# Performance work log

Hardware: AMD Instinct MI355X
Metric: run time of the kernel (lower is better)

## Reference

```python
import jax, jax.numpy as jnp
import numpy as np

N_SAMPLES = 16_777_216  # total surviving samples across all rays
N_RAY = 65_536          # number of rays


def setup_inputs() -> dict:
    key = jax.random.key(0)
    k1, k2 = jax.random.split(key)
    alpha = jax.random.uniform(k1, (N_SAMPLES,), dtype=jnp.float32)
    # sorted ray ids -> contiguous segments, as produced by create_full_step_id + masking
    ray_id = jnp.sort(jax.random.randint(k2, (N_SAMPLES,), 0, N_RAY, dtype=jnp.int32))
    return {"alpha": alpha, "ray_id": ray_id, "N_ray": N_RAY}


def _seg_prod_op(a, b):
    # segmented-product combine: reset the running product at segment starts
    va, fa = a
    vb, fb = b
    return jnp.where(fb, vb, va * vb), fa | fb


def reference(alpha, ray_id, N_ray):
    n = alpha.shape[0]
    one_minus_alpha = 1.0 - alpha + 1e-11                      # [n]
    is_start = jnp.concatenate(
        [jnp.ones((1,), jnp.bool_), ray_id[1:] != ray_id[:-1]]
    )                                                          # [n] segment starts
    # parallel segmented cumulative product (replaces the per-sample Python loop)
    cumprod, _ = jax.lax.associative_scan(_seg_prod_op, (one_minus_alpha, is_start))
    # NOTE: faithful to the source: transmittance is a global shift of cumprod
    # (cat([1, cumprod[:-1]])), NOT reset to 1 at each ray start.
    transmittance = jnp.concatenate([jnp.ones((1,), alpha.dtype), cumprod[:-1]])
    weights = alpha * transmittance                            # [n]
    # last sample index of each ray (ids are sorted, so max index == last write)
    last_idx = jnp.zeros((N_ray,), jnp.int32).at[ray_id].max(
        jnp.arange(n, dtype=jnp.int32)
    )                                                          # [N_ray]
    alphainv_last = cumprod[last_idx]                          # [N_ray]
    return weights, alphainv_last
```

## Files before the change

kernel.cpp:

```cpp
#include <hip/hip_runtime.h>
#include <stdint.h>


#define BLOCK 256
#define NWAVE (BLOCK / 64)
#define NJ 4
#define WELEM (64 * 4 * NJ)
#define CHUNK (NWAVE * WELEM)
#define LOOKW 1024

struct Pair { float v; int f; };

__device__ __forceinline__ Pair seg_combine(Pair a, Pair b) {
    Pair r;
    r.v = b.f ? b.v : (a.v * b.v);
    r.f = a.f | b.f;
    return r;
}

__device__ __forceinline__ Pair wave_scan_incl(Pair x, int lane) {
    #pragma unroll
    for (int off = 1; off < 64; off <<= 1) {
        Pair o;
        o.v = __shfl_up(x.v, off);
        o.f = __shfl_up(x.f, off);
        if (lane >= off) x = seg_combine(o, x);
    }
    return x;
}

__global__ void nerf_init(const float* __restrict__ alpha,
                          float* __restrict__ alphainv, int N_ray) {
    int i = blockIdx.x * blockDim.x + threadIdx.x;
    if (i < N_ray) alphainv[i] = (1.0f - alpha[0]) + 1e-11f;
}

__global__ __launch_bounds__(BLOCK, 4)
void nerf_fused(const float* __restrict__ alpha, const int* __restrict__ ray_id,
                float* __restrict__ weights, float* __restrict__ alphainv, int n) {
    __shared__ float s_wv[NWAVE];
    __shared__ int   s_wf[NWAVE];
    __shared__ int   s_rid[BLOCK];
    __shared__ float s_bv;
    __shared__ int   s_bf;

    const int c = blockIdx.x, t = threadIdx.x;
    const int lane = t & 63, w = t >> 6;
    const long bstart = (long)c * CHUNK;
    const long wbase  = bstart + (long)w * WELEM;

    float P0 = 1.0f;
    if (c > 0) {
        long wlo = bstart - LOOKW;
        Pair chain; chain.v = 1.0f; chain.f = 0;
        for (;;) {
            const long e0 = wlo + 4 * t;
            float4 av = *(const float4*)(alpha  + e0);
            int4   rv = *(const int4*)  (ray_id + e0);
            s_rid[t] = rv.w;
            __syncthreads();
            const int prev = (t == 0) ? ((wlo > 0) ? ray_id[wlo - 1] : -1) : s_rid[t - 1];
            Pair l;
            l.v = (1.0f - av.x) + 1e-11f; l.f = (rv.x != prev);
            { Pair e; e.v = (1.0f - av.y) + 1e-11f; e.f = (rv.y != rv.x); l = seg_combine(l, e); }
            { Pair e; e.v = (1.0f - av.z) + 1e-11f; e.f = (rv.z != rv.y); l = seg_combine(l, e); }
            { Pair e; e.v = (1.0f - av.w) + 1e-11f; e.f = (rv.w != rv.z); l = seg_combine(l, e); }
            #pragma unroll
            for (int off = 1; off < 64; off <<= 1) {
                Pair o;
                o.v = __shfl_down(l.v, off);
                o.f = __shfl_down(l.f, off);
                l = seg_combine(l, o);
            }
            if (lane == 0) { s_wv[w] = l.v; s_wf[w] = l.f; }
            __syncthreads();
            if (t == 0) {
                Pair acc; acc.v = s_wv[0]; acc.f = s_wf[0];
                #pragma unroll
                for (int ww = 1; ww < NWAVE; ++ww) {
                    Pair e; e.v = s_wv[ww]; e.f = s_wf[ww];
                    acc = seg_combine(acc, e);
                }
                s_bv = acc.v; s_bf = acc.f;
            }
            __syncthreads();
            Pair wagg; wagg.v = s_bv; wagg.f = s_bf;
            chain = seg_combine(wagg, chain);
            if (chain.f || wlo == 0) break;
            wlo -= LOOKW;
        }
        P0 = chain.v;
    }

    int last_r = -1;
    if (wbase > 0 && wbase - 1 < (long)n) last_r = ray_id[wbase - 1];

    float4 A[NJ]; int4 R[NJ]; Pair E[NJ]; int PR0[NJ];
    Pair wrun; wrun.v = 1.0f; wrun.f = 0;

    #pragma unroll
    for (int j = 0; j < NJ; ++j) {
        const long e0 = wbase + j * 256 + lane * 4;
        if (e0 + 4 <= (long)n) {
            A[j] = *(const float4*)(alpha  + e0);
            R[j] = *(const int4*)  (ray_id + e0);
        } else {
            float aa[4]; int rr[4];
            for (int k = 0; k < 4; ++k) {
                long g = e0 + k;
                aa[k] = (g < n) ? alpha[g]  : 0.0f;
                rr[k] = (g < n) ? ray_id[g] : -2;
            }
            A[j] = make_float4(aa[0], aa[1], aa[2], aa[3]);
            R[j] = make_int4(rr[0], rr[1], rr[2], rr[3]);
        }
        const float4 av = A[j]; const int4 rv = R[j];
        const bool b0 = e0 < n, b1 = e0 + 1 < n, b2 = e0 + 2 < n, b3 = e0 + 3 < n;
        const float om0 = b0 ? (1.0f - av.x) + 1e-11f : 1.0f;
        const float om1 = b1 ? (1.0f - av.y) + 1e-11f : 1.0f;
        const float om2 = b2 ? (1.0f - av.z) + 1e-11f : 1.0f;
        const float om3 = b3 ? (1.0f - av.w) + 1e-11f : 1.0f;
        const int up = __shfl_up(rv.w, 1);
        const int prev0 = (lane == 0) ? last_r : up;
        PR0[j] = prev0;
        const int f0 = b0 && (rv.x != prev0);
        const int f1 = b1 && (rv.y != rv.x);
        const int f2 = b2 && (rv.z != rv.y);
        const int f3 = b3 && (rv.w != rv.z);

        Pair l; l.v = om0; l.f = f0;
        { Pair e; e.v = om1; e.f = f1; l = seg_combine(l, e); }
        { Pair e; e.v = om2; e.f = f2; l = seg_combine(l, e); }
        { Pair e; e.v = om3; e.f = f3; l = seg_combine(l, e); }

        Pair ws = wave_scan_incl(l, lane);
        Pair wse;
        {
            float uv = __shfl_up(ws.v, 1);
            int   uf = __shfl_up(ws.f, 1);
            if (lane == 0) { wse.v = 1.0f; wse.f = 0; }
            else           { wse.v = uv;   wse.f = uf; }
        }
        E[j] = seg_combine(wrun, wse);
        Pair jag; jag.v = __shfl(ws.v, 63); jag.f = __shfl(ws.f, 63);
        wrun = seg_combine(wrun, jag);
        last_r = __shfl(rv.w, 63);
    }

    if (lane == 0) { s_wv[w] = wrun.v; s_wf[w] = wrun.f; }
    __syncthreads();

    Pair base; base.v = P0; base.f = (c > 0);
    for (int ww = 0; ww < w; ++ww) {
        Pair e; e.v = s_wv[ww]; e.f = s_wf[ww];
        base = seg_combine(base, e);
    }

    #pragma unroll
    for (int j = 0; j < NJ; ++j) {
        Pair P = seg_combine(base, E[j]);
        const float4 av = A[j]; const int4 rv = R[j];
        const long e0 = wbase + j * 256 + lane * 4;
        const bool b0 = e0 < n, b1 = e0 + 1 < n, b2 = e0 + 2 < n, b3 = e0 + 3 < n;
        const float om0 = b0 ? (1.0f - av.x) + 1e-11f : 1.0f;
        const float om1 = b1 ? (1.0f - av.y) + 1e-11f : 1.0f;
        const float om2 = b2 ? (1.0f - av.z) + 1e-11f : 1.0f;
        const float om3 = b3 ? (1.0f - av.w) + 1e-11f : 1.0f;
        const int prev0 = PR0[j];
        const int f0 = b0 && (rv.x != prev0);
        const int f1 = b1 && (rv.y != rv.x);
        const int f2 = b2 && (rv.z != rv.y);
        const int f3 = b3 && (rv.w != rv.z);

        float w0, w1, w2, w3;
        w0 = av.x * P.v;
        if (f0 && e0 > 0) alphainv[prev0] = P.v;
        { Pair e; e.v = om0; e.f = f0; P = seg_combine(P, e); }
        if (b0 && e0 == (long)n - 1) alphainv[rv.x] = P.v;
        w1 = av.y * P.v;
        if (f1) alphainv[rv.x] = P.v;
        { Pair e; e.v = om1; e.f = f1; P = seg_combine(P, e); }
        if (b1 && e0 + 1 == (long)n - 1) alphainv[rv.y] = P.v;
        w2 = av.z * P.v;
        if (f2) alphainv[rv.y] = P.v;
        { Pair e; e.v = om2; e.f = f2; P = seg_combine(P, e); }
        if (b2 && e0 + 2 == (long)n - 1) alphainv[rv.z] = P.v;
        w3 = av.w * P.v;
        if (f3) alphainv[rv.z] = P.v;
        { Pair e; e.v = om3; e.f = f3; P = seg_combine(P, e); }
        if (b3 && e0 + 3 == (long)n - 1) alphainv[rv.w] = P.v;

        if (e0 + 4 <= (long)n) {
            *(float4*)(weights + e0) = make_float4(w0, w1, w2, w3);
        } else {
            float ww4[4] = {w0, w1, w2, w3};
            for (int k = 0; k < 4; ++k) {
                long g = e0 + k;
                if (g < n) weights[g] = ww4[k];
            }
        }
    }
}

extern "C" void kernel_launch(void* const* d_in, const int* in_sizes, int n_in,
                              void* d_out, int out_size, void* d_ws, size_t ws_size,
                              hipStream_t stream) {
    const float* alpha  = (const float*)d_in[0];
    const int*   ray_id = (const int*)d_in[1];
    const int n     = in_sizes[0];
    const int N_ray = out_size - n;

    float* weights  = (float*)d_out;
    float* alphainv = weights + n;

    const int nchunks = (n + CHUNK - 1) / CHUNK;

    nerf_init<<<(N_ray + BLOCK - 1) / BLOCK, BLOCK, 0, stream>>>(alpha, alphainv, N_ray);
    nerf_fused<<<nchunks, BLOCK, 0, stream>>>(alpha, ray_id, weights, alphainv, n);
}
```

Before: 179.3 us.

## Encode segment flag in float sign bit and use wave-level lookback

Packs each (value, segment-start flag) pair into one float by storing the flag in the sign bit. Each scan step then needs one shuffle instead of two, and fewer registers. The block-wide lookback with shared memory and three barriers becomes a per-wave lookback over a 256-element window, with no barriers, that every wave computes redundantly. The main-chunk loads are hoisted ahead of the lookback so their latency overlaps it. The risk is more redundant lookback loads per wave, and relying on the one-minus-alpha values always being positive.

```diff
diff --git a/kernel.cpp b/kernel.cpp
--- a/kernel.cpp
+++ b/kernel.cpp
@@ -7,26 +7,10 @@
 #define NJ 4
 #define WELEM (64 * 4 * NJ)
 #define CHUNK (NWAVE * WELEM)
-#define LOOKW 1024
+#define WIN 256
 
-struct Pair { float v; int f; };
-
-__device__ __forceinline__ Pair seg_combine(Pair a, Pair b) {
-    Pair r;
-    r.v = b.f ? b.v : (a.v * b.v);
-    r.f = a.f | b.f;
-    return r;
-}
-
-__device__ __forceinline__ Pair wave_scan_incl(Pair x, int lane) {
-    #pragma unroll
-    for (int off = 1; off < 64; off <<= 1) {
-        Pair o;
-        o.v = __shfl_up(x.v, off);
-        o.f = __shfl_up(x.f, off);
-        if (lane >= off) x = seg_combine(o, x);
-    }
-    return x;
+__device__ __forceinline__ float comb(float a, float b) {
+    return (__float_as_int(b) < 0) ? b : a * b;
 }
 
 __global__ void nerf_init(const float* __restrict__ alpha,
@@ -39,73 +23,29 @@
 void nerf_fused(const float* __restrict__ alpha, const int* __restrict__ ray_id,
                 float* __restrict__ weights, float* __restrict__ alphainv, int n) {
     __shared__ float s_wv[NWAVE];
-    __shared__ int   s_wf[NWAVE];
-    __shared__ int   s_rid[BLOCK];
-    __shared__ float s_bv;
-    __shared__ int   s_bf;
 
     const int c = blockIdx.x, t = threadIdx.x;
     const int lane = t & 63, w = t >> 6;
     const long bstart = (long)c * CHUNK;
     const long wbase  = bstart + (long)w * WELEM;
 
-    float P0 = 1.0f;
+    long wlo = bstart - WIN;
+    float4 wav; int4 wrv;
     if (c > 0) {
-        long wlo = bstart - LOOKW;
-        Pair chain; chain.v = 1.0f; chain.f = 0;
-        for (;;) {
-            const long e0 = wlo + 4 * t;
-            float4 av = *(const float4*)(alpha  + e0);
-            int4   rv = *(const int4*)  (ray_id + e0);
-            s_rid[t] = rv.w;
-            __syncthreads();
-            const int prev = (t == 0) ? ((wlo > 0) ? ray_id[wlo - 1] : -1) : s_rid[t - 1];
-            Pair l;
-            l.v = (1.0f - av.x) + 1e-11f; l.f = (rv.x != prev);
-            { Pair e; e.v = (1.0f - av.y) + 1e-11f; e.f = (rv.y != rv.x); l = seg_combine(l, e); }
-            { Pair e; e.v = (1.0f - av.z) + 1e-11f; e.f = (rv.z != rv.y); l = seg_combine(l, e); }
-            { Pair e; e.v = (1.0f - av.w) + 1e-11f; e.f = (rv.w != rv.z); l = seg_combine(l, e); }
-            #pragma unroll
-            for (int off = 1; off < 64; off <<= 1) {
-                Pair o;
-                o.v = __shfl_down(l.v, off);
-                o.f = __shfl_down(l.f, off);
-                l = seg_combine(l, o);
-            }
-            if (lane == 0) { s_wv[w] = l.v; s_wf[w] = l.f; }
-            __syncthreads();
-            if (t == 0) {
-                Pair acc; acc.v = s_wv[0]; acc.f = s_wf[0];
-                #pragma unroll
-                for (int ww = 1; ww < NWAVE; ++ww) {
-                    Pair e; e.v = s_wv[ww]; e.f = s_wf[ww];
-                    acc = seg_combine(acc, e);
-                }
-                s_bv = acc.v; s_bf = acc.f;
-            }
-            __syncthreads();
-            Pair wagg; wagg.v = s_bv; wagg.f = s_bf;
-            chain = seg_combine(wagg, chain);
-            if (chain.f || wlo == 0) break;
-            wlo -= LOOKW;
-        }
-        P0 = chain.v;
+        wav = *(const float4*)(alpha  + wlo + lane * 4);
+        wrv = *(const int4*)  (ray_id + wlo + lane * 4);
     }
 
-    int last_r = -1;
-    if (wbase > 0 && wbase - 1 < (long)n) last_r = ray_id[wbase - 1];
-
-    float4 A[NJ]; int4 R[NJ]; Pair E[NJ]; int PR0[NJ];
-    Pair wrun; wrun.v = 1.0f; wrun.f = 0;
-
+    float4 A[NJ]; int4 R[NJ];
     #pragma unroll
     for (int j = 0; j < NJ; ++j) {
-        const long e0 = wbase + j * 256 + lane * 4;
+        const long e0 = wbase + (long)j * 256 + lane * 4;
         if (e0 + 4 <= (long)n) {
             A[j] = *(const float4*)(alpha  + e0);
             R[j] = *(const int4*)  (ray_id + e0);
         } else {
             float aa[4]; int rr[4];
+            #pragma unroll
             for (int k = 0; k < 4; ++k) {
                 long g = e0 + k;
                 aa[k] = (g < n) ? alpha[g]  : 0.0f;
@@ -114,53 +54,84 @@
             A[j] = make_float4(aa[0], aa[1], aa[2], aa[3]);
             R[j] = make_int4(rr[0], rr[1], rr[2], rr[3]);
         }
+    }
+    int last_r = -1;
+    if (wbase > 0 && wbase - 1 < (long)n) last_r = ray_id[wbase - 1];
+
+    float P0 = 1.0f;
+    if (c > 0) {
+        float chain = 1.0f;
+        for (;;) {
+            int pw = __shfl_up(wrv.w, 1);
+            if (lane == 0) pw = (wlo > 0) ? ray_id[wlo - 1] : -1;
+            const float om0 = (1.0f - wav.x) + 1e-11f;
+            const float om1 = (1.0f - wav.y) + 1e-11f;
+            const float om2 = (1.0f - wav.z) + 1e-11f;
+            const float om3 = (1.0f - wav.w) + 1e-11f;
+            const float s0 = (wrv.x != pw)    ? -om0 : om0;
+            const float s1 = (wrv.y != wrv.x) ? -om1 : om1;
+            const float s2 = (wrv.z != wrv.y) ? -om2 : om2;
+            const float s3 = (wrv.w != wrv.z) ? -om3 : om3;
+            float l = comb(comb(comb(s0, s1), s2), s3);
+            #pragma unroll
+            for (int off = 1; off < 64; off <<= 1) {
+                float o = __shfl_down(l, off);
+                l = comb(l, o);
+            }
+            float wagg = __shfl(l, 0);
+            chain = comb(wagg, chain);
+            if (__float_as_int(chain) < 0 || wlo == 0) break;
+            wlo -= WIN;
+            wav = *(const float4*)(alpha  + wlo + lane * 4);
+            wrv = *(const int4*)  (ray_id + wlo + lane * 4);
+        }
+        P0 = chain;
+    }
+
+    float E[NJ]; int PR0[NJ];
+    float wrun = 1.0f;
+    #pragma unroll
+    for (int j = 0; j < NJ; ++j) {
+        const long e0 = wbase + (long)j * 256 + lane * 4;
         const float4 av = A[j]; const int4 rv = R[j];
         const bool b0 = e0 < n, b1 = e0 + 1 < n, b2 = e0 + 2 < n, b3 = e0 + 3 < n;
         const float om0 = b0 ? (1.0f - av.x) + 1e-11f : 1.0f;
         const float om1 = b1 ? (1.0f - av.y) + 1e-11f : 1.0f;
         const float om2 = b2 ? (1.0f - av.z) + 1e-11f : 1.0f;
         const float om3 = b3 ? (1.0f - av.w) + 1e-11f : 1.0f;
-        const int up = __shfl_up(rv.w, 1);
-        const int prev0 = (lane == 0) ? last_r : up;
+        int pw = __shfl_up(rv.w, 1);
+        const int prev0 = (lane == 0) ? last_r : pw;
         PR0[j] = prev0;
-        const int f0 = b0 && (rv.x != prev0);
-        const int f1 = b1 && (rv.y != rv.x);
-        const int f2 = b2 && (rv.z != rv.y);
-        const int f3 = b3 && (rv.w != rv.z);
+        const float s0 = (b0 && rv.x != prev0) ? -om0 : om0;
+        const float s1 = (b1 && rv.y != rv.x)  ? -om1 : om1;
+        const float s2 = (b2 && rv.z != rv.y)  ? -om2 : om2;
+        const float s3 = (b3 && rv.w != rv.z)  ? -om3 : om3;
+        float l = comb(comb(comb(s0, s1), s2), s3);
 
-        Pair l; l.v = om0; l.f = f0;
-        { Pair e; e.v = om1; e.f = f1; l = seg_combine(l, e); }
-        { Pair e; e.v = om2; e.f = f2; l = seg_combine(l, e); }
-        { Pair e; e.v = om3; e.f = f3; l = seg_combine(l, e); }
-
-        Pair ws = wave_scan_incl(l, lane);
-        Pair wse;
-        {
-            float uv = __shfl_up(ws.v, 1);
-            int   uf = __shfl_up(ws.f, 1);
-            if (lane == 0) { wse.v = 1.0f; wse.f = 0; }
-            else           { wse.v = uv;   wse.f = uf; }
+        float ws = l;
+        #pragma unroll
+        for (int off = 1; off < 64; off <<= 1) {
+            float o = __shfl_up(ws, off);
+            if (lane >= off) ws = comb(o, ws);
         }
-        E[j] = seg_combine(wrun, wse);
-        Pair jag; jag.v = __shfl(ws.v, 63); jag.f = __shfl(ws.f, 63);
-        wrun = seg_combine(wrun, jag);
+        float wse = __shfl_up(ws, 1);
+        if (lane == 0) wse = 1.0f;
+        E[j] = comb(wrun, wse);
+        wrun = comb(wrun, __shfl(ws, 63));
         last_r = __shfl(rv.w, 63);
     }
 
-    if (lane == 0) { s_wv[w] = wrun.v; s_wf[w] = wrun.f; }
+    if (lane == 0) s_wv[w] = wrun;
     __syncthreads();
 
-    Pair base; base.v = P0; base.f = (c > 0);
-    for (int ww = 0; ww < w; ++ww) {
-        Pair e; e.v = s_wv[ww]; e.f = s_wf[ww];
-        base = seg_combine(base, e);
-    }
+    float base = P0;
+    for (int ww = 0; ww < w; ++ww) base = comb(base, s_wv[ww]);
 
     #pragma unroll
     for (int j = 0; j < NJ; ++j) {
-        Pair P = seg_combine(base, E[j]);
+        float P = comb(base, E[j]);
         const float4 av = A[j]; const int4 rv = R[j];
-        const long e0 = wbase + j * 256 + lane * 4;
+        const long e0 = wbase + (long)j * 256 + lane * 4;
         const bool b0 = e0 < n, b1 = e0 + 1 < n, b2 = e0 + 2 < n, b3 = e0 + 3 < n;
         const float om0 = b0 ? (1.0f - av.x) + 1e-11f : 1.0f;
         const float om1 = b1 ? (1.0f - av.y) + 1e-11f : 1.0f;
@@ -172,23 +143,27 @@
         const int f2 = b2 && (rv.z != rv.y);
         const int f3 = b3 && (rv.w != rv.z);
 
-        float w0, w1, w2, w3;
-        w0 = av.x * P.v;
-        if (f0 && e0 > 0) alphainv[prev0] = P.v;
-        { Pair e; e.v = om0; e.f = f0; P = seg_combine(P, e); }
-        if (b0 && e0 == (long)n - 1) alphainv[rv.x] = P.v;
-        w1 = av.y * P.v;
-        if (f1) alphainv[rv.x] = P.v;
-        { Pair e; e.v = om1; e.f = f1; P = seg_combine(P, e); }
-        if (b1 && e0 + 1 == (long)n - 1) alphainv[rv.y] = P.v;
-        w2 = av.z * P.v;
-        if (f2) alphainv[rv.y] = P.v;
-        { Pair e; e.v = om2; e.f = f2; P = seg_combine(P, e); }
-        if (b2 && e0 + 2 == (long)n - 1) alphainv[rv.z] = P.v;
-        w3 = av.w * P.v;
-        if (f3) alphainv[rv.z] = P.v;
-        { Pair e; e.v = om3; e.f = f3; P = seg_combine(P, e); }
-        if (b3 && e0 + 3 == (long)n - 1) alphainv[rv.w] = P.v;
+        float w0, w1, w2, w3, trans;
+        trans = fabsf(P);
+        w0 = av.x * trans;
+        if (f0 && e0 > 0) alphainv[prev0] = trans;
+        P = comb(P, f0 ? -om0 : om0);
+        if (b0 && e0 == (long)n - 1) alphainv[rv.x] = fabsf(P);
+        trans = fabsf(P);
+        w1 = av.y * trans;
+        if (f1) alphainv[rv.x] = trans;
+        P = comb(P, f1 ? -om1 : om1);
+        if (b1 && e0 + 1 == (long)n - 1) alphainv[rv.y] = fabsf(P);
+        trans = fabsf(P);
+        w2 = av.z * trans;
+        if (f2) alphainv[rv.y] = trans;
+        P = comb(P, f2 ? -om2 : om2);
+        if (b2 && e0 + 2 == (long)n - 1) alphainv[rv.z] = fabsf(P);
+        trans = fabsf(P);
+        w3 = av.w * trans;
+        if (f3) alphainv[rv.z] = trans;
+        P = comb(P, f3 ? -om3 : om3);
+        if (b3 && e0 + 3 == (long)n - 1) alphainv[rv.w] = fabsf(P);
 
         if (e0 + 4 <= (long)n) {
             *(float4*)(weights + e0) = make_float4(w0, w1, w2, w3);
```

Result: faster. 175.6 us (-2.1%).
